# Optimization experiments

Hardware: AMD Instinct MI355X
Metric: run time of the kernel (lower is better)

Reference implementation:

```python
import jax, jax.numpy as jnp
import numpy as np

D = 1024      # model dim (used for theta exponent and 1/sqrt(d) scale)
D_H = 128     # head dim


def make_theta():
    # theta[i] = 10 ** (-2*(i-1)/d), each value repeated twice -> length d_H
    i = np.repeat(np.arange(D_H // 2), 2)
    return jnp.asarray(10.0 ** (-2.0 * (i - 1) / D), dtype=jnp.float32)


def rotation(x, theta):
    # x: [B, T, d_H]; positions are 1..T (source uses arange(1, T+1))
    B, T, dh = x.shape
    idx = jnp.arange(1, T + 1, dtype=x.dtype)[:, None]          # [T, 1]
    ang = idx * theta[None, :]                                   # [T, d_H]
    cos, sin = jnp.cos(ang), jnp.sin(ang)
    # pairwise swap with sign: (x0, x1) -> (x1, -x0)
    x2 = x.reshape(B, T, dh // 2, 2)
    swapped = jnp.stack([x2[..., 1], -x2[..., 0]], axis=-1).reshape(B, T, dh)
    return x * cos + swapped * sin


def setup_inputs() -> dict:
    key = jax.random.key(0)
    kx, kq, kk, kv = jax.random.split(key, 4)
    B, T = 4, 2048
    scale = 1.0 / np.sqrt(D)
    return {
        "x": jax.random.normal(kx, (B, T, D), dtype=jnp.float32),
        "Wq": jax.random.normal(kq, (D_H, D), dtype=jnp.float32) * scale,
        "Wk": jax.random.normal(kk, (D_H, D), dtype=jnp.float32) * scale,
        "Wv": jax.random.normal(kv, (D_H, D), dtype=jnp.float32) * scale,
        "theta": make_theta(),
    }


def reference(x, Wq, Wk, Wv, theta):
    B, T, d = x.shape
    Q = jnp.einsum('btd,hd->bth', x, Wq)
    K = jnp.einsum('btd,hd->bth', x, Wk)
    V = jnp.einsum('btd,hd->bth', x, Wv)
    Q = rotation(Q, theta)
    K = rotation(K, theta)
    # scale uses model dim d (not d_H), as in the source
    scores = jnp.einsum('bqh,bkh->bqk', Q, K) * (d ** -0.5)
    causal = jnp.tril(jnp.ones((T, T), dtype=bool))
    scores = jnp.where(causal, scores, -jnp.inf)
    attn = jax.nn.softmax(scores, axis=-1)
    return jnp.einsum('bqk,bkh->bqh', attn, V)
```

## Files before the change

kernel.cpp:

```cpp
#include <hip/hip_runtime.h>
#include <math.h>

#define T_SEQ 2048
#define D_MODEL 1024
#define DH 128
#define SLOTS 288
#define FRAG_B 262144

typedef __bf16 bfx8 __attribute__((ext_vector_type(8)));
typedef float f32x4 __attribute__((ext_vector_type(4)));

union U16x8 { uint4 u4; unsigned int ui[4]; unsigned short us[8]; __bf16 bf[8]; bfx8 v; };

__device__ inline uint4 cvt8u(float4 a, float4 b) {
    U16x8 u;
    u.bf[0] = (__bf16)a.x; u.bf[1] = (__bf16)a.y; u.bf[2] = (__bf16)a.z; u.bf[3] = (__bf16)a.w;
    u.bf[4] = (__bf16)b.x; u.bf[5] = (__bf16)b.y; u.bf[6] = (__bf16)b.z; u.bf[7] = (__bf16)b.w;
    return u.u4;
}

__device__ inline int slot_base32(int qt) {
    int g = qt >> 3, j = qt & 7;
    return 4 * g * (g + 1) + j * (g + 1);
}

__global__ __launch_bounds__(256) void prep_kernel(
    const float* __restrict__ x,
    const float* __restrict__ Wq, const float* __restrict__ Wk,
    const float* __restrict__ Wv,
    __bf16* __restrict__ xF, __bf16* __restrict__ WF, int nxb)
{
    const int bi = blockIdx.x;
    const int tid = threadIdx.x;

    if (bi < nxb) {
        __shared__ __align__(16) unsigned short Xs[64 * 72];
        const int m0 = (bi >> 4) * 64;
        const int k0 = (bi & 15) * 64;
        const int row = tid >> 2, cs = (tid & 3) * 16;
        const float* xp = x + (size_t)(m0 + row) * D_MODEL + k0 + cs;
        float4 a0 = *(const float4*)xp;
        float4 a1 = *(const float4*)(xp + 4);
        float4 a2 = *(const float4*)(xp + 8);
        float4 a3 = *(const float4*)(xp + 12);
        *(uint4*)&Xs[row * 72 + cs]     = cvt8u(a0, a1);
        *(uint4*)&Xs[row * 72 + cs + 8] = cvt8u(a2, a3);
        __syncthreads();
        const int L = tid & 63;
        #pragma unroll
        for (int rr = 0; rr < 2; ++rr) {
            const int fid = rr * 4 + (tid >> 6);
            const int mtl = fid >> 1, kcl = fid & 1;
            uint4 d = *(const uint4*)&Xs[(mtl * 16 + (L & 15)) * 72 + kcl * 32 + (L >> 4) * 8];
            const size_t frag = (size_t)((m0 >> 4) + mtl) * 32 + (k0 >> 5) + kcl;
            *(uint4*)&xF[frag * 512 + L * 8] = d;
        }
    } else {
        const int i = (bi - nxb) * 256 + tid;
        const int wsel = i >> 14;
        const int i2 = i & 16383;
        const int kc = i2 >> 9, j = (i2 >> 6) & 7, ln = i2 & 63;
        const int lo = ln & 15, quad = ln >> 4;
        const float* src = (wsel == 0) ? Wq : (wsel == 1) ? Wk : Wv;
        const float* p = src + (size_t)(j * 16 + lo) * D_MODEL + kc * 32 + quad * 8;
        float4 a = *(const float4*)p;
        float4 b = *(const float4*)(p + 4);
        *(uint4*)&WF[(size_t)((wsel * 32 + kc) * 8 + j) * 512 + ln * 8] = cvt8u(a, b);
    }
}

__global__ __launch_bounds__(64) void qkv_kernel(
    const __bf16* __restrict__ xF, const __bf16* __restrict__ WF,
    const float* __restrict__ theta,
    __bf16* __restrict__ QF, __bf16* __restrict__ KF, __bf16* __restrict__ VF)
{
    __shared__ __align__(16) unsigned short T[32 * 136];

    const int bx = blockIdx.x;
    const int ln = threadIdx.x;
    const int lo = ln & 15, quad = ln >> 4;

    if (bx < 2048) {
        const int wsel01 = bx >> 10;
        const int sub = (bx >> 8) & 3;
        const int iq = sub >> 1, jh = sub & 1;
        const int mt = bx & 255;
        const int mt16 = mt * 2 + iq;

        const __bf16* WFp = WF + (size_t)wsel01 * (32 * 8 * 512) + (size_t)jh * (4 * 512);
        const size_t xb = (size_t)mt16 * 32;

        bfx8 xA = *(const bfx8*)&xF[(xb + 0) * 512 + ln * 8];
        bfx8 xB = *(const bfx8*)&xF[(xb + 1) * 512 + ln * 8];
        bfx8 wA[4], wB[4];
        #pragma unroll
        for (int jl = 0; jl < 4; ++jl) {
            wA[jl] = *(const bfx8*)&WFp[(size_t)jl * 512 + ln * 8];
            wB[jl] = *(const bfx8*)&WFp[(size_t)(8 + jl) * 512 + ln * 8];
        }

        f32x4 acc[4];
        #pragma unroll
        for (int jl = 0; jl < 4; ++jl) acc[jl] = (f32x4)(0.f);

        for (int kc = 0; kc < 32; kc += 2) {
            const int kpA = (kc + 2 < 32) ? kc + 2 : kc;
            #pragma unroll
            for (int jl = 0; jl < 4; ++jl) {
                acc[jl] = __builtin_amdgcn_mfma_f32_16x16x32_bf16(xA, wA[jl], acc[jl], 0, 0, 0);
                wA[jl] = *(const bfx8*)&WFp[((size_t)kpA * 8 + jl) * 512 + ln * 8];
            }
            xA = *(const bfx8*)&xF[(xb + kpA) * 512 + ln * 8];
            const int kpB = (kc + 3 < 32) ? kc + 3 : kc + 1;
            #pragma unroll
            for (int jl = 0; jl < 4; ++jl) {
                acc[jl] = __builtin_amdgcn_mfma_f32_16x16x32_bf16(xB, wB[jl], acc[jl], 0, 0, 0);
                wB[jl] = *(const bfx8*)&WFp[((size_t)kpB * 8 + jl) * 512 + ln * 8];
            }
            xB = *(const bfx8*)&xF[(xb + kpB) * 512 + ln * 8];
        }

        const int b = mt16 >> 7;
        const int t16 = mt16 & 127;
        const int mloc16 = t16 * 16;
        __bf16* dstP = (wsel01 == 0 ? QF : KF) + (size_t)b * FRAG_B;

        #pragma unroll
        for (int jl = 0; jl < 4; ++jl) {
            const int j = jh * 4 + jl;
            const int h = j * 16 + lo;
            const float th = theta[h];
            #pragma unroll
            for (int r = 0; r < 4; ++r) {
                const int pos = mloc16 + quad * 4 + r + 1;
                float v = acc[jl][r];
                float partner = __shfl_xor(v, 1, 64);
                float ang = (float)pos * th;
                float rev = ang * 0.15915494309189535f;
                rev -= floorf(rev);
                float sn = __builtin_amdgcn_sinf(rev);
                float cs = __builtin_amdgcn_cosf(rev);
                float res = (h & 1) ? (v * cs - partner * sn)
                                    : (v * cs + partner * sn);
                U16x8 u; u.bf[0] = (__bf16)res;
                T[(quad * 4 + r) * 136 + h] = u.us[0];
            }
        }
        #pragma unroll
        for (int c4l = 0; c4l < 2; ++c4l) {
            const int c4 = jh * 2 + c4l;
            uint4 d = *(const uint4*)&T[(ln & 15) * 136 + c4 * 32 + (ln >> 4) * 8];
            *(uint4*)&dstP[(size_t)(t16 * 4 + c4) * 512 + ln * 8] = d;
        }
    } else {
        const int r2 = bx - 2048;
        const int jh = r2 >> 8;
        const int mt = r2 & 255;
        const int mt16 = mt * 2;

        const __bf16* WFp = WF + (size_t)2 * (32 * 8 * 512) + (size_t)jh * (4 * 512);
        const size_t xb0 = (size_t)mt16 * 32, xb1 = xb0 + 32;

        bfx8 xA[2], xB[2], wA[4], wB[4];
        xA[0] = *(const bfx8*)&xF[(xb0 + 0) * 512 + ln * 8];
        xA[1] = *(const bfx8*)&xF[(xb1 + 0) * 512 + ln * 8];
        xB[0] = *(const bfx8*)&xF[(xb0 + 1) * 512 + ln * 8];
        xB[1] = *(const bfx8*)&xF[(xb1 + 1) * 512 + ln * 8];
        #pragma unroll
        for (int jl = 0; jl < 4; ++jl) {
            wA[jl] = *(const bfx8*)&WFp[(size_t)jl * 512 + ln * 8];
            wB[jl] = *(const bfx8*)&WFp[(size_t)(8 + jl) * 512 + ln * 8];
        }

        f32x4 acc[2][4];
        #pragma unroll
        for (int iq = 0; iq < 2; ++iq)
            #pragma unroll
            for (int jl = 0; jl < 4; ++jl) acc[iq][jl] = (f32x4)(0.f);

        for (int kc = 0; kc < 32; kc += 2) {
            const int kpA = (kc + 2 < 32) ? kc + 2 : kc;
            #pragma unroll
            for (int jl = 0; jl < 4; ++jl) {
                acc[0][jl] = __builtin_amdgcn_mfma_f32_16x16x32_bf16(xA[0], wA[jl], acc[0][jl], 0, 0, 0);
                acc[1][jl] = __builtin_amdgcn_mfma_f32_16x16x32_bf16(xA[1], wA[jl], acc[1][jl], 0, 0, 0);
                wA[jl] = *(const bfx8*)&WFp[((size_t)kpA * 8 + jl) * 512 + ln * 8];
            }
            xA[0] = *(const bfx8*)&xF[(xb0 + kpA) * 512 + ln * 8];
            xA[1] = *(const bfx8*)&xF[(xb1 + kpA) * 512 + ln * 8];
            const int kpB = (kc + 3 < 32) ? kc + 3 : kc + 1;
            #pragma unroll
            for (int jl = 0; jl < 4; ++jl) {
                acc[0][jl] = __builtin_amdgcn_mfma_f32_16x16x32_bf16(xB[0], wB[jl], acc[0][jl], 0, 0, 0);
                acc[1][jl] = __builtin_amdgcn_mfma_f32_16x16x32_bf16(xB[1], wB[jl], acc[1][jl], 0, 0, 0);
                wB[jl] = *(const bfx8*)&WFp[((size_t)kpB * 8 + jl) * 512 + ln * 8];
            }
            xB[0] = *(const bfx8*)&xF[(xb0 + kpB) * 512 + ln * 8];
            xB[1] = *(const bfx8*)&xF[(xb1 + kpB) * 512 + ln * 8];
        }

        const int b = mt >> 6;
        const int kt32 = mt & 63;
        #pragma unroll
        for (int iq = 0; iq < 2; ++iq)
            #pragma unroll
            for (int jl = 0; jl < 4; ++jl) {
                const int j = jh * 4 + jl;
                #pragma unroll
                for (int r = 0; r < 4; ++r) {
                    U16x8 u; u.bf[0] = (__bf16)acc[iq][jl][r];
                    T[(iq * 16 + quad * 4 + r) * 136 + j * 16 + lo] = u.us[0];
                }
            }
        __bf16* dstP = VF + (size_t)b * FRAG_B;
        #pragma unroll
        for (int jl = 0; jl < 4; ++jl) {
            const int j = jh * 4 + jl;
            U16x8 u;
            #pragma unroll
            for (int e = 0; e < 8; ++e)
                u.us[e] = T[((ln >> 4) * 8 + e) * 136 + j * 16 + (ln & 15)];
            *(uint4*)&dstP[(size_t)(kt32 * 8 + j) * 512 + ln * 8] = u.u4;
        }
    }
}

__global__ __launch_bounds__(64) void attn_partial_kernel(
    const __bf16* __restrict__ QF, const __bf16* __restrict__ KF,
    const __bf16* __restrict__ VF,
    __bf16* __restrict__ Opb, float* __restrict__ Ll)
{
    const int qt = blockIdx.x, c = blockIdx.y, b = blockIdx.z;
    const int qbase = qt * 32;
    const int kstart = c << 8;
    if (kstart > qbase) return;
    const int nt = min(8, (qbase + 32 - kstart) >> 5);

    __shared__ __align__(16) unsigned short Pw[2 * 640];

    const int ln = threadIdx.x;
    const int lo = ln & 15, quad = ln >> 4;
    const int hi8 = quad * 8;

    const __bf16* QFb = QF + (size_t)b * FRAG_B;
    const __bf16* KFb = KF + (size_t)b * FRAG_B;
    const __bf16* VFb = VF + (size_t)b * FRAG_B;

    bfx8 qf[2][4];
    #pragma unroll
    for (int iq = 0; iq < 2; ++iq)
        #pragma unroll
        for (int c4 = 0; c4 < 4; ++c4)
            qf[iq][c4] = *(const bfx8*)&QFb[(size_t)((qt * 2 + iq) * 4 + c4) * 512 + ln * 8];

    f32x4 O[2][8];
    #pragma unroll
    for (int iq = 0; iq < 2; ++iq)
        #pragma unroll
        for (int j = 0; j < 8; ++j) O[iq][j] = (f32x4)(0.f);
    float lsum[2][4];
    #pragma unroll
    for (int iq = 0; iq < 2; ++iq)
        #pragma unroll
        for (int r = 0; r < 4; ++r) lsum[iq][r] = 0.f;

    bfx8 kcur[2][4], knxt[2][4];
    #pragma unroll
    for (int jj = 0; jj < 2; ++jj)
        #pragma unroll
        for (int c4 = 0; c4 < 4; ++c4)
            kcur[jj][c4] = *(const bfx8*)&KFb[(size_t)(((kstart >> 4) + jj) * 4 + c4) * 512 + ln * 8];

    for (int kt = 0; kt < nt; ++kt) {
        const int k0 = kstart + kt * 32;
        bfx8 vf[8];
        #pragma unroll
        for (int j = 0; j < 8; ++j)
            vf[j] = *(const bfx8*)&VFb[(size_t)((k0 >> 5) * 8 + j) * 512 + ln * 8];
        if (kt + 1 < nt) {
            const int kn16 = (k0 + 32) >> 4;
            #pragma unroll
            for (int jj = 0; jj < 2; ++jj)
                #pragma unroll
                for (int c4 = 0; c4 < 4; ++c4)
                    knxt[jj][c4] = *(const bfx8*)&KFb[(size_t)((kn16 + jj) * 4 + c4) * 512 + ln * 8];
        }

        f32x4 s4[2][2];
        #pragma unroll
        for (int iq = 0; iq < 2; ++iq)
            #pragma unroll
            for (int jj = 0; jj < 2; ++jj) s4[iq][jj] = (f32x4)(0.f);
        #pragma unroll
        for (int c4 = 0; c4 < 4; ++c4)
            #pragma unroll
            for (int iq = 0; iq < 2; ++iq)
                #pragma unroll
                for (int jj = 0; jj < 2; ++jj)
                    s4[iq][jj] = __builtin_amdgcn_mfma_f32_16x16x32_bf16(qf[iq][c4], kcur[jj][c4], s4[iq][jj], 0, 0, 0);

        const bool needMask = (k0 + 31 > qbase);
        #pragma unroll
        for (int iq = 0; iq < 2; ++iq)
            #pragma unroll
            for (int jj = 0; jj < 2; ++jj)
                #pragma unroll
                for (int r = 0; r < 4; ++r) {
                    const int col = k0 + jj * 16 + lo;
                    const int row = qbase + iq * 16 + quad * 4 + r;
                    float p = __expf(s4[iq][jj][r] * 0.03125f);
                    if (needMask && col > row) p = 0.f;
                    lsum[iq][r] += p;
                    U16x8 u; u.bf[0] = (__bf16)p;
                    Pw[iq * 640 + (quad * 4 + r) * 40 + jj * 16 + lo] = u.us[0];
                }

        bfx8 pf0 = *(const bfx8*)&Pw[lo * 40 + hi8];
        bfx8 pf1 = *(const bfx8*)&Pw[640 + lo * 40 + hi8];
        #pragma unroll
        for (int j = 0; j < 8; ++j) {
            O[0][j] = __builtin_amdgcn_mfma_f32_16x16x32_bf16(pf0, vf[j], O[0][j], 0, 0, 0);
            O[1][j] = __builtin_amdgcn_mfma_f32_16x16x32_bf16(pf1, vf[j], O[1][j], 0, 0, 0);
        }

        #pragma unroll
        for (int jj = 0; jj < 2; ++jj)
            #pragma unroll
            for (int c4 = 0; c4 < 4; ++c4) kcur[jj][c4] = knxt[jj][c4];
    }

    #pragma unroll
    for (int off = 1; off < 16; off <<= 1)
        #pragma unroll
        for (int iq = 0; iq < 2; ++iq)
            #pragma unroll
            for (int r = 0; r < 4; ++r) lsum[iq][r] += __shfl_xor(lsum[iq][r], off, 64);

    const size_t sb = (size_t)b * SLOTS + slot_base32(qt) + c;
    #pragma unroll
    for (int iq = 0; iq < 2; ++iq)
        #pragma unroll
        for (int j = 0; j < 8; ++j) {
            U16x8 u;
            u.bf[0] = (__bf16)O[iq][j][0]; u.bf[1] = (__bf16)O[iq][j][1];
            u.bf[2] = (__bf16)O[iq][j][2]; u.bf[3] = (__bf16)O[iq][j][3];
            *(uint2*)&Opb[((sb * 2 + iq) * 8 + j) * 256 + ln * 4] = make_uint2(u.ui[0], u.ui[1]);
        }
    if (lo == 0) {
        #pragma unroll
        for (int iq = 0; iq < 2; ++iq)
            #pragma unroll
            for (int r = 0; r < 4; ++r)
                Ll[sb * 32 + iq * 16 + quad * 4 + r] = lsum[iq][r];
    }
}

__global__ __launch_bounds__(128) void attn_merge_kernel(
    const __bf16* __restrict__ Opb, const float* __restrict__ Ll,
    float* __restrict__ out)
{
    const int qt = blockIdx.x, b = blockIdx.y, j = blockIdx.z;
    const int g = qt >> 3, nc = g + 1;
    const size_t base = (size_t)b * SLOTS + slot_base32(qt);

    __shared__ float Lsh[8][32];
    const int tid = threadIdx.x;
    const int iq = tid >> 6, ln = tid & 63;
    const int lo = ln & 15, quad = ln >> 4;

    for (int idx = tid; idx < nc * 32; idx += 128)
        Lsh[idx >> 5][idx & 31] = Ll[(base + (idx >> 5)) * 32 + (idx & 31)];
    __syncthreads();

    float acc[4] = {0.f, 0.f, 0.f, 0.f};
    for (int cc = 0; cc < nc; ++cc) {
        uint2 d = *(const uint2*)&Opb[(((base + cc) * 2 + iq) * 8 + j) * 256 + ln * 4];
        U16x8 u; u.ui[0] = d.x; u.ui[1] = d.y;
        #pragma unroll
        for (int r = 0; r < 4; ++r) acc[r] += (float)u.bf[r];
    }

    #pragma unroll
    for (int r = 0; r < 4; ++r) {
        const int row = iq * 16 + quad * 4 + r;
        float l = 0.f;
        for (int cc = 0; cc < nc; ++cc) l += Lsh[cc][row];
        out[((size_t)b * T_SEQ + qt * 32 + row) * DH + j * 16 + lo] = acc[r] / l;
    }
}

extern "C" void kernel_launch(void* const* d_in, const int* in_sizes, int n_in,
                              void* d_out, int out_size, void* d_ws, size_t ws_size,
                              hipStream_t stream) {
    const float* x     = (const float*)d_in[0];
    const float* Wq    = (const float*)d_in[1];
    const float* Wk    = (const float*)d_in[2];
    const float* Wv    = (const float*)d_in[3];
    const float* theta = (const float*)d_in[4];
    float* out = (float*)d_out;

    const int M = in_sizes[0] / D_MODEL;
    const int B = M / T_SEQ;

    __bf16* xF  = (__bf16*)d_ws;
    __bf16* WF  = xF + (size_t)M * D_MODEL;
    __bf16* QF  = WF + (size_t)3 * 32 * 8 * 512;
    __bf16* KF  = QF + (size_t)B * FRAG_B;
    __bf16* VF  = KF + (size_t)B * FRAG_B;
    __bf16* Opb = VF + (size_t)B * FRAG_B;
    float*  Ll  = (float*)(Opb + (size_t)B * SLOTS * 2 * 8 * 256);

    const int nxb = (M / 64) * 16;
    prep_kernel<<<dim3(nxb + 192), 256, 0, stream>>>(x, Wq, Wk, Wv, xF, WF, nxb);
    qkv_kernel<<<dim3(2048 + 512), 64, 0, stream>>>(xF, WF, theta, QF, KF, VF);
    attn_partial_kernel<<<dim3(T_SEQ / 32, 8, B), 64, 0, stream>>>(QF, KF, VF, Opb, Ll);
    attn_merge_kernel<<<dim3(T_SEQ / 32, B, 8), 128, 0, stream>>>(Opb, Ll, out);
}
```

Before: 123.7 us.

## Split key tiles of each attention block across two waves with LDS reduction

```diff
diff --git a/kernel.cpp b/kernel.cpp
--- a/kernel.cpp
+++ b/kernel.cpp
@@ -225,7 +225,7 @@
     }
 }
 
-__global__ __launch_bounds__(64) void attn_partial_kernel(
+__global__ __launch_bounds__(128) void attn_partial_kernel(
     const __bf16* __restrict__ QF, const __bf16* __restrict__ KF,
     const __bf16* __restrict__ VF,
     __bf16* __restrict__ Opb, float* __restrict__ Ll)
@@ -236,9 +236,13 @@
     if (kstart > qbase) return;
     const int nt = min(8, (qbase + 32 - kstart) >> 5);
 
-    __shared__ __align__(16) unsigned short Pw[2 * 640];
-
-    const int ln = threadIdx.x;
+    __shared__ __align__(16) unsigned short Pw[2][1280];
+    __shared__ float RedO[2 * 8 * 4 * 64];
+    __shared__ float RedL[2 * 4 * 64];
+
+    const int tid = threadIdx.x;
+    const int w = tid >> 6;
+    const int ln = tid & 63;
     const int lo = ln & 15, quad = ln >> 4;
     const int hi8 = quad * 8;
 
@@ -265,20 +269,23 @@
         for (int r = 0; r < 4; ++r) lsum[iq][r] = 0.f;
 
     bfx8 kcur[2][4], knxt[2][4];
-    #pragma unroll
-    for (int jj = 0; jj < 2; ++jj)
-        #pragma unroll
-        for (int c4 = 0; c4 < 4; ++c4)
-            kcur[jj][c4] = *(const bfx8*)&KFb[(size_t)(((kstart >> 4) + jj) * 4 + c4) * 512 + ln * 8];
-
-    for (int kt = 0; kt < nt; ++kt) {
+    {
+        const int kf0 = (kstart + w * 32) >> 4;
+        #pragma unroll
+        for (int jj = 0; jj < 2; ++jj)
+            #pragma unroll
+            for (int c4 = 0; c4 < 4; ++c4)
+                kcur[jj][c4] = *(const bfx8*)&KFb[(size_t)((kf0 + jj) * 4 + c4) * 512 + ln * 8];
+    }
+
+    for (int kt = w; kt < nt; kt += 2) {
         const int k0 = kstart + kt * 32;
         bfx8 vf[8];
         #pragma unroll
         for (int j = 0; j < 8; ++j)
             vf[j] = *(const bfx8*)&VFb[(size_t)((k0 >> 5) * 8 + j) * 512 + ln * 8];
-        if (kt + 1 < nt) {
-            const int kn16 = (k0 + 32) >> 4;
+        if (kt + 2 < nt) {
+            const int kn16 = (k0 + 64) >> 4;
             #pragma unroll
             for (int jj = 0; jj < 2; ++jj)
                 #pragma unroll
@@ -312,11 +319,11 @@
                     if (needMask && col > row) p = 0.f;
                     lsum[iq][r] += p;
                     U16x8 u; u.bf[0] = (__bf16)p;
-                    Pw[iq * 640 + (quad * 4 + r) * 40 + jj * 16 + lo] = u.us[0];
+                    Pw[w][iq * 640 + (quad * 4 + r) * 40 + jj * 16 + lo] = u.us[0];
                 }
 
-        bfx8 pf0 = *(const bfx8*)&Pw[lo * 40 + hi8];
-        bfx8 pf1 = *(const bfx8*)&Pw[640 + lo * 40 + hi8];
+        bfx8 pf0 = *(const bfx8*)&Pw[w][lo * 40 + hi8];
+        bfx8 pf1 = *(const bfx8*)&Pw[w][640 + lo * 40 + hi8];
         #pragma unroll
         for (int j = 0; j < 8; ++j) {
             O[0][j] = __builtin_amdgcn_mfma_f32_16x16x32_bf16(pf0, vf[j], O[0][j], 0, 0, 0);
@@ -336,22 +343,52 @@
             #pragma unroll
             for (int r = 0; r < 4; ++r) lsum[iq][r] += __shfl_xor(lsum[iq][r], off, 64);
 
-    const size_t sb = (size_t)b * SLOTS + slot_base32(qt) + c;
-    #pragma unroll
-    for (int iq = 0; iq < 2; ++iq)
-        #pragma unroll
-        for (int j = 0; j < 8; ++j) {
-            U16x8 u;
-            u.bf[0] = (__bf16)O[iq][j][0]; u.bf[1] = (__bf16)O[iq][j][1];
-            u.bf[2] = (__bf16)O[iq][j][2]; u.bf[3] = (__bf16)O[iq][j][3];
-            *(uint2*)&Opb[((sb * 2 + iq) * 8 + j) * 256 + ln * 4] = make_uint2(u.ui[0], u.ui[1]);
-        }
-    if (lo == 0) {
+    if (w == 1) {
+        #pragma unroll
+        for (int iq = 0; iq < 2; ++iq)
+            #pragma unroll
+            for (int j = 0; j < 8; ++j)
+                #pragma unroll
+                for (int r = 0; r < 4; ++r)
+                    RedO[((iq * 8 + j) * 4 + r) * 64 + ln] = O[iq][j][r];
         #pragma unroll
         for (int iq = 0; iq < 2; ++iq)
             #pragma unroll
             for (int r = 0; r < 4; ++r)
-                Ll[sb * 32 + iq * 16 + quad * 4 + r] = lsum[iq][r];
+                RedL[(iq * 4 + r) * 64 + ln] = lsum[iq][r];
+    }
+    __syncthreads();
+    if (w == 0) {
+        #pragma unroll
+        for (int iq = 0; iq < 2; ++iq)
+            #pragma unroll
+            for (int j = 0; j < 8; ++j)
+                #pragma unroll
+                for (int r = 0; r < 4; ++r)
+                    O[iq][j][r] += RedO[((iq * 8 + j) * 4 + r) * 64 + ln];
+        #pragma unroll
+        for (int iq = 0; iq < 2; ++iq)
+            #pragma unroll
+            for (int r = 0; r < 4; ++r)
+                lsum[iq][r] += RedL[(iq * 4 + r) * 64 + ln];
+
+        const size_t sb = (size_t)b * SLOTS + slot_base32(qt) + c;
+        #pragma unroll
+        for (int iq = 0; iq < 2; ++iq)
+            #pragma unroll
+            for (int j = 0; j < 8; ++j) {
+                U16x8 u;
+                u.bf[0] = (__bf16)O[iq][j][0]; u.bf[1] = (__bf16)O[iq][j][1];
+                u.bf[2] = (__bf16)O[iq][j][2]; u.bf[3] = (__bf16)O[iq][j][3];
+                *(uint2*)&Opb[((sb * 2 + iq) * 8 + j) * 256 + ln * 4] = make_uint2(u.ui[0], u.ui[1]);
+            }
+        if (lo == 0) {
+            #pragma unroll
+            for (int iq = 0; iq < 2; ++iq)
+                #pragma unroll
+                for (int r = 0; r < 4; ++r)
+                    Ll[sb * 32 + iq * 16 + quad * 4 + r] = lsum[iq][r];
+        }
     }
 }
 
@@ -413,6 +450,6 @@
     const int nxb = (M / 64) * 16;
     prep_kernel<<<dim3(nxb + 192), 256, 0, stream>>>(x, Wq, Wk, Wv, xF, WF, nxb);
     qkv_kernel<<<dim3(2048 + 512), 64, 0, stream>>>(xF, WF, theta, QF, KF, VF);
-    attn_partial_kernel<<<dim3(T_SEQ / 32, 8, B), 64, 0, stream>>>(QF, KF, VF, Opb, Ll);
+    attn_partial_kernel<<<dim3(T_SEQ / 32, 8, B), 128, 0, stream>>>(QF, KF, VF, Opb, Ll);
     attn_merge_kernel<<<dim3(T_SEQ / 32, B, 8), 128, 0, stream>>>(Opb, Ll, out);
 }
```

Result: no change. 123.2 us (-0.4%).
